# Optimization experiments

Measured on AMD Instinct MI355X. Metric: run time of the kernel, lower is better.

The kernel has to match this reference:

```python
import jax, jax.numpy as jnp
import numpy as np
import itertools

EPS = 1e-3  # BatchNorm1d eps in the original module
N_VOX = 100000


def _build_sparse_structure():
    """Build realistic clustered voxel coords, a 3x3x3 submanifold neighbor
    table (spconv rulebook equivalent), and the unique-merge mapping used by
    sum_duplicates. All index structure is constant (non-differentiable)."""
    rng = np.random.default_rng(0)
    B, Z, Y, X = 2, 40, 1600, 1408  # sparse_shape = grid_size[::-1] + [1,0,0]
    offs01 = np.array(list(itertools.product([0, 1], repeat=3)), dtype=np.int64)
    coords = []
    for b in range(B):
        base = np.stack([rng.integers(0, Z - 1, 13000),
                         rng.integers(0, Y - 1, 13000),
                         rng.integers(0, X - 1, 13000)], 1)
        exp = (base[:, None, :] + offs01[None]).reshape(-1, 3)  # clustered voxels
        coords.append(np.concatenate([np.full((len(exp), 1), b, np.int64), exp], 1))
    coords = np.unique(np.concatenate(coords, 0), axis=0)[:N_VOX]
    assert len(coords) == N_VOX
    # lexicographic unique order => encoded keys are sorted ascending
    key = ((coords[:, 0] * Z + coords[:, 1]) * Y + coords[:, 2]) * X + coords[:, 3]
    offs27 = np.array(list(itertools.product([-1, 0, 1], repeat=3)), np.int64)
    nc = coords[:, None, 1:] + offs27[None]  # [N,27,3]
    inb = (nc >= 0).all(-1) & (nc[..., 0] < Z) & (nc[..., 1] < Y) & (nc[..., 2] < X)
    nk = ((coords[:, None, 0] * Z + nc[..., 0]) * Y + nc[..., 1]) * X + nc[..., 2]
    pos = np.searchsorted(key, nk).clip(0, N_VOX - 1)
    valid = inb & (key[pos] == nk)
    nbr_idx = np.where(valid, pos, -1).astype(np.int32)  # [N,27], -1 = empty
    # second sparse tensor: half its voxels coincide, half are shifted in x
    coords2 = coords.copy()
    coords2[::2, 3] = np.minimum(coords2[::2, 3] + 1, X - 1)
    comb = np.concatenate([coords, coords2], 0)
    uniq, inv = np.unique(comb, axis=0, return_inverse=True)
    return nbr_idx, inv.astype(np.int32), int(len(uniq))


def setup_inputs() -> dict:
    nbr_idx, seg_ids, num_segments = _build_sparse_structure()
    key = jax.random.key(0)
    ks = jax.random.split(key, 6)
    C = 16
    return {
        'voxel_features': jax.random.normal(ks[0], (N_VOX, C), jnp.float32),
        'feat2': jax.random.normal(ks[1], (N_VOX, C), jnp.float32),
        'W0': jax.random.normal(ks[2], (27, C, 16), jnp.float32) * 0.1,
        'g0': jnp.ones((16,), jnp.float32),
        'b0': jnp.zeros((16,), jnp.float32),
        'W1': jax.random.normal(ks[3], (27, 16, 16), jnp.float32) * 0.1,
        'g1': jnp.ones((16,), jnp.float32),
        'b1': jnp.zeros((16,), jnp.float32),
        'Wobo': jax.random.normal(ks[4], (16, 16), jnp.float32) * 0.1,
        'bobo': jnp.zeros((16,), jnp.float32),
        'Wf': jax.random.normal(ks[5], (16, 128), jnp.float32) * 0.1,
        'bf': jnp.zeros((128,), jnp.float32),
        'nbr_idx': jnp.asarray(nbr_idx),
        'seg_ids': jnp.asarray(seg_ids),
        'num_segments': num_segments,
    }


def _subm_bn_relu(x, W, g, b, nbr_idx):
    """Submanifold 3x3x3 sparse conv (gather->GEMM) + BatchNorm1d + ReLU."""
    N = x.shape[0]
    xp = jnp.concatenate([x, jnp.zeros((1, x.shape[1]), x.dtype)], 0)  # pad row
    idx = jnp.where(nbr_idx < 0, N, nbr_idx)  # missing neighbor -> zero row
    y = jnp.einsum('nkc,kco->no', xp[idx], W)  # [N,27,Cin] x [27,Cin,Cout]
    mu = y.mean(0)
    var = y.var(0)
    return jax.nn.relu((y - mu) * jax.lax.rsqrt(var + EPS) * g + b)


def reference(voxel_features, feat2, W0, g0, b0, W1, g1, b1, Wobo, bobo, Wf, bf,
              nbr_idx, seg_ids, num_segments):
    # level-0 conv_input + conv1 (subm conv, BN, ReLU)
    h = _subm_bn_relu(voxel_features, W0, g0, b0, nbr_idx)
    h = _subm_bn_relu(h, W1, g1, b1, nbr_idx)
    # obo_* 1x1 sparse conv on the second branch (plain matmul + bias)
    t2 = feat2 @ Wobo + bobo
    # sum_duplicates: merge coincident sparse indices by summing features
    comb = jnp.concatenate([h, t2], 0)  # [2N,16]
    merged = jax.ops.segment_sum(comb, seg_ids, num_segments=num_segments)
    # final 1x1 sparse conv
    return merged @ Wf + bf  # [U,128]
```

## Files before the change

kernel.cpp:

```cpp
#include <hip/hip_runtime.h>

#define BN_EPS 1e-3f
#define STATC  32
#define MBLK   128

using bfrag  = __attribute__((ext_vector_type(8))) short;
using f32x4v = __attribute__((ext_vector_type(4))) float;
using i32x4v = __attribute__((ext_vector_type(4))) int;

__device__ __forceinline__ unsigned short f2bf(float f) {
    union { float f; unsigned u; } v; v.f = f;
    unsigned r = v.u + 0x7FFFu + ((v.u >> 16) & 1u);
    return (unsigned short)(r >> 16);
}

__global__ __launch_bounds__(256)
void prep_kernel(const float* __restrict__ vf,
                 const float* __restrict__ W0, const float* __restrict__ W1,
                 const float* __restrict__ Wf, const int* __restrict__ seg,
                 unsigned short* __restrict__ xb0,
                 unsigned short* __restrict__ Wb0, unsigned short* __restrict__ Wb1,
                 unsigned short* __restrict__ Wfb,
                 float* __restrict__ stats,
                 int* __restrict__ hidx, int* __restrict__ t2s, int N)
{
    int t = blockIdx.x * 256 + threadIdx.x;
    int TA = 2 * (N + 1);
    unsigned short tmp[8];
    if (t < TA) {
        int n = t >> 1, h = t & 1;
        if (n < N) {
            const f32x4v* yr = (const f32x4v*)(vf + (size_t)n * 16 + h * 8);
            f32x4v v0 = __builtin_nontemporal_load(yr);
            f32x4v v1 = __builtin_nontemporal_load(yr + 1);
#pragma unroll
            for (int j = 0; j < 4; ++j) { tmp[j] = f2bf(v0[j]); tmp[4 + j] = f2bf(v1[j]); }
        } else {
#pragma unroll
            for (int j = 0; j < 8; ++j) tmp[j] = 0;
        }
        *(int4*)(xb0 + (size_t)n * 16 + h * 8) = *(int4*)tmp;
        return;
    }
    t -= TA;
    if (t < 2 * 14 * 64) {
        int w = t >= 896;
        int l = t - w * 896;
        int s = l >> 6, lane = l & 63;
        int q = lane >> 4, n = lane & 15;
        int tap = 2 * s + (q >> 1);
        int cb  = (q & 1) * 8;
        const float* W = w ? W1 : W0;
        unsigned short* Wb = w ? Wb1 : Wb0;
#pragma unroll
        for (int j = 0; j < 8; ++j)
            tmp[j] = (tap < 27) ? f2bf(W[((size_t)(tap * 16 + cb + j)) * 16 + n]) : 0;
        *(int4*)(Wb + (size_t)l * 8) = *(int4*)tmp;
        return;
    }
    t -= 2 * 14 * 64;
    if (t < 512) {
        int ct = t >> 6, lane = t & 63;
        int q = lane >> 4, n = lane & 15;
#pragma unroll
        for (int j = 0; j < 8; ++j)
            tmp[j] = (q < 2) ? f2bf(Wf[(size_t)(q * 8 + j) * 128 + ct * 16 + n]) : 0;
        *(int4*)(Wfb + (size_t)t * 8) = *(int4*)tmp;
        return;
    }
    t -= 512;
    if (t < 2 * STATC * 32) { stats[t] = 0.f; return; }
    t -= 2 * STATC * 32;
    if (t < N) { hidx[seg[t]] = t; return; }
    t -= N;
    if (t < N) {
        int s = seg[N + t];
        if (t == 0 || seg[N + t - 1] != s) t2s[s] = t;
    }
}

__global__ __launch_bounds__(256)
void conv_stats_kernel(const unsigned short* __restrict__ xb,
                       const unsigned short* __restrict__ Wb,
                       const int* __restrict__ nbr,
                       float* __restrict__ y,
                       float* __restrict__ statsC,
                       int N)
{
    __shared__ __align__(16) int   sNbr[64 * 27];
    __shared__ __align__(16) float sY[64 * 16];
    __shared__ float sred[32];
    int tid = threadIdx.x;
    if (tid < 32) sred[tid] = 0.f;

    int gb = blockIdx.x * 1728;
    int NT = N * 27;
    if (gb + 1728 <= NT) {
#pragma unroll
        for (int i = 0; i < 2; ++i) {
            int t4 = i * 256 + tid;
            if (t4 < 432) {
                i32x4v v = __builtin_nontemporal_load((const i32x4v*)(nbr + gb) + t4);
                *(i32x4v*)(sNbr + t4 * 4) = v;
            }
        }
    } else {
#pragma unroll
        for (int i = 0; i < 7; ++i) {
            int t = i * 256 + tid;
            if (t < 1728) {
                int g2 = gb + t;
                sNbr[t] = (g2 < NT) ? __builtin_nontemporal_load(nbr + g2) : -1;
            }
        }
    }
    __syncthreads();

    int lane = tid & 63, wib = tid >> 6;
    int q = lane >> 4, m = lane & 15;
    int c0   = (q & 1) * 8;
    int tpar = q >> 1;
    int lvox = wib * 16 + m;

    int idx[14];
#pragma unroll
    for (int s = 0; s < 14; ++s) {
        int tap = 2 * s + tpar;
        int id  = (tap < 27) ? sNbr[lvox * 27 + tap] : -1;
        idx[s]  = (id >= 0) ? id : N;
    }

    f32x4v acc = {0.f, 0.f, 0.f, 0.f};
#pragma unroll
    for (int s = 0; s < 14; ++s) {
        bfrag a = *(const bfrag*)(xb + (size_t)idx[s] * 16 + c0);
        bfrag b = *(const bfrag*)(Wb + ((size_t)s * 64 + lane) * 8);
        acc = __builtin_amdgcn_mfma_f32_16x16x32_bf16(a, b, acc, 0, 0, 0);
    }

    int o = lane & 15;
#pragma unroll
    for (int i = 0; i < 4; ++i)
        sY[(wib * 16 + q * 4 + i) * 16 + o] = acc[i];

    float s  = acc[0] + acc[1] + acc[2] + acc[3];
    float qq = acc[0] * acc[0] + acc[1] * acc[1] + acc[2] * acc[2] + acc[3] * acc[3];
    s  += __shfl_xor(s, 16);  s  += __shfl_xor(s, 32);
    qq += __shfl_xor(qq, 16); qq += __shfl_xor(qq, 32);
    if (lane < 16) {
        atomicAdd(&sred[lane], s);
        atomicAdd(&sred[16 + lane], qq);
    }
    __syncthreads();

    {
        int row = blockIdx.x * 64 + (tid >> 2);
        if (row < N)
            *(f32x4v*)(y + (size_t)row * 16 + (tid & 3) * 4) =
                *(const f32x4v*)(sY + (size_t)(tid >> 2) * 16 + (tid & 3) * 4);
    }
    if (tid < 32)
        atomicAdd(&statsC[(blockIdx.x & (STATC - 1)) * 32 + tid], sred[tid]);
}

__global__ __launch_bounds__(256)
void bnrelu_cvt_kernel(const float* __restrict__ y0, const float* __restrict__ statsC,
                       const float* __restrict__ g, const float* __restrict__ b,
                       float invN, unsigned short* __restrict__ xb, int N)
{
    __shared__ float sred[32];
    __shared__ float sSc[16], sSh[16];
    int tid = threadIdx.x;
    if (tid < 32) {
        float v = 0.f;
#pragma unroll
        for (int k = 0; k < STATC; ++k) v += statsC[k * 32 + tid];
        sred[tid] = v;
    }
    __syncthreads();
    if (tid < 16) {
        float mu  = sred[tid] * invN;
        float var = sred[16 + tid] * invN - mu * mu;
        float sc  = g[tid] * rsqrtf(var + BN_EPS);
        sSc[tid] = sc;
        sSh[tid] = b[tid] - mu * sc;
    }
    __syncthreads();

    int t = blockIdx.x * 256 + tid;
    if (t >= (N + 1) * 2) return;
    int n = t >> 1, h = t & 1;
    unsigned short tmp[8];
    if (n < N) {
        const f32x4v* yr4 = (const f32x4v*)(y0 + (size_t)n * 16 + h * 8);
        f32x4v v0 = __builtin_nontemporal_load(yr4);
        f32x4v v1 = __builtin_nontemporal_load(yr4 + 1);
#pragma unroll
        for (int j = 0; j < 4; ++j) {
            int c = h * 8 + j;
            tmp[j]     = f2bf(fmaxf(fmaf(v0[j], sSc[c], sSh[c]), 0.f));
            tmp[4 + j] = f2bf(fmaxf(fmaf(v1[j], sSc[c + 4], sSh[c + 4]), 0.f));
        }
    } else {
#pragma unroll
        for (int j = 0; j < 8; ++j) tmp[j] = 0;
    }
    *(int4*)(xb + (size_t)n * 16 + h * 8) = *(int4*)tmp;
}

__global__ __launch_bounds__(256)
void merge_final_kernel(const float* __restrict__ y1, const float* __restrict__ statsC,
                        const float* __restrict__ g, const float* __restrict__ b,
                        float invN,
                        const float* __restrict__ feat2, const float* __restrict__ Wobo,
                        const float* __restrict__ bobo,
                        const int* __restrict__ seg,
                        const int* __restrict__ hidx, const int* __restrict__ t2s,
                        const unsigned short* __restrict__ Wfb,
                        const float* __restrict__ bf,
                        float* __restrict__ out, int N, int U)
{
    __shared__ unsigned short smA[MBLK * 16];
    __shared__ float sred[32];
    __shared__ float sSc[16], sSh[16];
    int tid = threadIdx.x;
    int u0  = blockIdx.x * MBLK;

    if (tid < 32) {
        float v = 0.f;
#pragma unroll
        for (int k = 0; k < STATC; ++k) v += statsC[k * 32 + tid];
        sred[tid] = v;
    }
    __syncthreads();
    if (tid < 16) {
        float mu  = sred[tid] * invN;
        float var = sred[16 + tid] * invN - mu * mu;
        float sc  = g[tid] * rsqrtf(var + BN_EPS);
        sSc[tid] = sc;
        sSh[tid] = b[tid] - mu * sc;
    }
    __syncthreads();

    {
        int sl = tid >> 1, half = tid & 1;
        int u  = u0 + sl;
        bool valid = u < U;
        int uc = valid ? u : 0;
        int hi = hidx[uc];
        int r  = t2s[uc];
        bool hasH = valid && (unsigned)hi < (unsigned)N && seg[hi] == u;
        bool hasT = valid && (unsigned)r  < (unsigned)N && seg[N + r] == u;

        size_t hoff = (size_t)(hasH ? hi : 0) * 16 + half * 8;
        f32x4v yv0 = *(const f32x4v*)(y1 + hoff);
        f32x4v yv1 = *(const f32x4v*)(y1 + hoff + 4);

        float m[8];
#pragma unroll
        for (int j = 0; j < 8; ++j) m[j] = 0.f;
        if (hasH) {
#pragma unroll
            for (int j = 0; j < 4; ++j) {
                int c = half * 8 + j;
                m[j]     = fmaxf(fmaf(yv0[j], sSc[c],     sSh[c]),     0.f);
                m[4 + j] = fmaxf(fmaf(yv1[j], sSc[c + 4], sSh[c + 4]), 0.f);
            }
        }
        if (hasT) {
            float S[16];
#pragma unroll
            for (int c = 0; c < 16; ++c) S[c] = 0.f;
            do {
                const f32x4v* fr = (const f32x4v*)(feat2 + (size_t)r * 16);
                f32x4v f0 = __builtin_nontemporal_load(fr);
                f32x4v f1 = __builtin_nontemporal_load(fr + 1);
                f32x4v f2 = __builtin_nontemporal_load(fr + 2);
                f32x4v f3 = __builtin_nontemporal_load(fr + 3);
#pragma unroll
                for (int c = 0; c < 4; ++c) {
                    S[c] += f0[c]; S[4 + c] += f1[c];
                    S[8 + c] += f2[c]; S[12 + c] += f3[c];
                }
                ++r;
            } while (r < N && seg[N + r] == u);
            float a2[8];
#pragma unroll
            for (int j = 0; j < 8; ++j) a2[j] = bobo[half * 8 + j];
#pragma unroll
            for (int c = 0; c < 16; ++c) {
                float xc = S[c];
                const float* wr = Wobo + c * 16 + half * 8;
#pragma unroll
                for (int j = 0; j < 8; ++j) a2[j] = fmaf(xc, wr[j], a2[j]);
            }
#pragma unroll
            for (int j = 0; j < 8; ++j) m[j] += a2[j];
        }
        unsigned short tb[8];
#pragma unroll
        for (int j = 0; j < 8; ++j) tb[j] = f2bf(m[j]);
        *(int4*)(smA + (size_t)tid * 8) = *(int4*)tb;
    }
    __syncthreads();

    int lane = tid & 63, w = tid >> 6;
    int q = lane >> 4, n = lane & 15;
#pragma unroll
    for (int rt = 0; rt < 2; ++rt) {
        int row0 = w * 32 + rt * 16;
        bfrag a = {0, 0, 0, 0, 0, 0, 0, 0};
        if (q < 2)
            a = *(const bfrag*)(smA + ((size_t)(row0 + n) * 16 + q * 8));
#pragma unroll
        for (int ct = 0; ct < 8; ++ct) {
            bfrag bb = *(const bfrag*)(Wfb + ((size_t)(ct * 64 + lane)) * 8);
            f32x4v acc = {0.f, 0.f, 0.f, 0.f};
            acc = __builtin_amdgcn_mfma_f32_16x16x32_bf16(a, bb, acc, 0, 0, 0);
            int col = ct * 16 + n;
            float bv = bf[col];
#pragma unroll
            for (int i = 0; i < 4; ++i) {
                int u = u0 + row0 + q * 4 + i;
                if (u < U) out[(size_t)u * 128 + col] = acc[i] + bv;
            }
        }
    }
}

extern "C" void kernel_launch(void* const* d_in, const int* in_sizes, int n_in,
                              void* d_out, int out_size, void* d_ws, size_t ws_size,
                              hipStream_t stream)
{
    const float* vf    = (const float*)d_in[0];
    const float* feat2 = (const float*)d_in[1];
    const float* W0    = (const float*)d_in[2];
    const float* g0    = (const float*)d_in[3];
    const float* b0    = (const float*)d_in[4];
    const float* W1    = (const float*)d_in[5];
    const float* g1    = (const float*)d_in[6];
    const float* b1    = (const float*)d_in[7];
    const float* Wobo  = (const float*)d_in[8];
    const float* bobo  = (const float*)d_in[9];
    const float* Wf    = (const float*)d_in[10];
    const float* bf    = (const float*)d_in[11];
    const int*   nbr   = (const int*)d_in[12];
    const int*   seg   = (const int*)d_in[13];

    int N = in_sizes[0] / 16;
    int U = out_size / 128;

    float* out = (float*)d_out;
    float* ws  = (float*)d_ws;

    int gbConv = (N + 63) / 64;

    float* y0     = ws;
    float* y1     = y0 + (size_t)N * 16;
    float* statsA = y1 + (size_t)N * 16;
    float* statsB = statsA + STATC * 32;
    unsigned short* xb0 = (unsigned short*)(statsB + STATC * 32);
    unsigned short* xb1 = xb0 + (size_t)(N + 1) * 16;
    unsigned short* Wb0 = xb1 + (size_t)(N + 1) * 16;
    unsigned short* Wb1 = Wb0 + 14 * 64 * 8;
    unsigned short* Wfb = Wb1 + 14 * 64 * 8;
    int* hidx = (int*)(Wfb + 8 * 64 * 8);
    int* t2s  = hidx + U;

    float invN  = 1.f / (float)N;
    int thrPrep = 2 * (N + 1) + 2 * 14 * 64 + 512 + 2 * STATC * 32 + 2 * N;
    int gbPrep  = (thrPrep + 255) / 256;
    int gbCvt   = ((N + 1) * 2 + 255) / 256;
    int gbMerge = (U + MBLK - 1) / MBLK;

    prep_kernel<<<gbPrep, 256, 0, stream>>>(vf, W0, W1, Wf, seg, xb0, Wb0, Wb1,
                                            Wfb, statsA, hidx, t2s, N);
    conv_stats_kernel<<<gbConv, 256, 0, stream>>>(xb0, Wb0, nbr, y0, statsA, N);
    bnrelu_cvt_kernel<<<gbCvt, 256, 0, stream>>>(y0, statsA, g0, b0, invN, xb1, N);
    conv_stats_kernel<<<gbConv, 256, 0, stream>>>(xb1, Wb1, nbr, y1, statsB, N);
    merge_final_kernel<<<gbMerge, 256, 0, stream>>>(y1, statsB, g1, b1, invN,
                                                    feat2, Wobo, bobo, seg,
                                                    hidx, t2s, Wfb, bf, out, N, U);
}
```

Measured before the change: 150.0 us.

## Pre-swizzle neighbor table into per-lane MFMA order in prep kernel

The prep kernel now rewrites the neighbor index table once into a tiled layout matching each lane's MFMA tap order, with missing neighbors already mapped to the zero row. Both conv kernels then load their 16 indices with four vector loads instead of staging the raw table through shared memory and a barrier. This removes per-conv LDS staging and remapping work, and the raw table is read once instead of twice. In exchange it adds an extra workspace buffer and a write pass in prep, and it leaves a now-unneeded __syncthreads in the conv kernel.

Measured after the change: 156.2 us. 4.2% more time.

```diff
diff --git a/kernel.cpp b/kernel.cpp
--- a/kernel.cpp
+++ b/kernel.cpp
@@ -14,15 +14,18 @@
     return (unsigned short)(r >> 16);
 }
 
+
 __global__ __launch_bounds__(256)
 void prep_kernel(const float* __restrict__ vf,
                  const float* __restrict__ W0, const float* __restrict__ W1,
                  const float* __restrict__ Wf, const int* __restrict__ seg,
+                 const int* __restrict__ nbr,
                  unsigned short* __restrict__ xb0,
                  unsigned short* __restrict__ Wb0, unsigned short* __restrict__ Wb1,
                  unsigned short* __restrict__ Wfb,
                  float* __restrict__ stats,
-                 int* __restrict__ hidx, int* __restrict__ t2s, int N)
+                 int* __restrict__ hidx, int* __restrict__ t2s,
+                 int* __restrict__ nbr2, int nTile, int N)
 {
     int t = blockIdx.x * 256 + threadIdx.x;
     int TA = 2 * (N + 1);
@@ -76,59 +79,57 @@
     if (t < N) {
         int s = seg[N + t];
         if (t == 0 || seg[N + t - 1] != s) t2s[s] = t;
+        return;
+    }
+    t -= N;
+    if (t < nTile * 512) {
+        int lane32 = t & 31;
+        int tpar = lane32 >> 4, m = lane32 & 15;
+        int r2 = t >> 5;
+        int k = r2 & 3; r2 >>= 2;
+        int wib = r2 & 3; int blk = r2 >> 2;
+        int row = blk * 64 + wib * 16 + m;
+        int vals[4];
+#pragma unroll
+        for (int j = 0; j < 4; ++j) {
+            int tap = 8 * k + 2 * j + tpar;
+            int id = -1;
+            if (row < N && tap < 27)
+                id = __builtin_nontemporal_load(nbr + (size_t)row * 27 + tap);
+            vals[j] = (id >= 0) ? id : N;
+        }
+        *(int4*)(nbr2 + (size_t)t * 4) = *(int4*)vals;
     }
 }
 
 __global__ __launch_bounds__(256)
 void conv_stats_kernel(const unsigned short* __restrict__ xb,
                        const unsigned short* __restrict__ Wb,
-                       const int* __restrict__ nbr,
+                       const int* __restrict__ nbr2,
                        float* __restrict__ y,
                        float* __restrict__ statsC,
                        int N)
 {
-    __shared__ __align__(16) int   sNbr[64 * 27];
     __shared__ __align__(16) float sY[64 * 16];
     __shared__ float sred[32];
     int tid = threadIdx.x;
     if (tid < 32) sred[tid] = 0.f;
 
-    int gb = blockIdx.x * 1728;
-    int NT = N * 27;
-    if (gb + 1728 <= NT) {
-#pragma unroll
-        for (int i = 0; i < 2; ++i) {
-            int t4 = i * 256 + tid;
-            if (t4 < 432) {
-                i32x4v v = __builtin_nontemporal_load((const i32x4v*)(nbr + gb) + t4);
-                *(i32x4v*)(sNbr + t4 * 4) = v;
-            }
-        }
-    } else {
-#pragma unroll
-        for (int i = 0; i < 7; ++i) {
-            int t = i * 256 + tid;
-            if (t < 1728) {
-                int g2 = gb + t;
-                sNbr[t] = (g2 < NT) ? __builtin_nontemporal_load(nbr + g2) : -1;
-            }
-        }
-    }
-    __syncthreads();
-
     int lane = tid & 63, wib = tid >> 6;
     int q = lane >> 4, m = lane & 15;
     int c0   = (q & 1) * 8;
     int tpar = q >> 1;
-    int lvox = wib * 16 + m;
-
-    int idx[14];
-#pragma unroll
-    for (int s = 0; s < 14; ++s) {
-        int tap = 2 * s + tpar;
-        int id  = (tap < 27) ? sNbr[lvox * 27 + tap] : -1;
-        idx[s]  = (id >= 0) ? id : N;
-    }
+
+    const int* nb = nbr2 +
+        ((((size_t)blockIdx.x * 4 + wib) * 4) * 32 + tpar * 16 + m) * 4;
+    int idx[16];
+#pragma unroll
+    for (int k = 0; k < 4; ++k) {
+        i32x4v v = *(const i32x4v*)(nb + (size_t)k * 128);
+        idx[4 * k + 0] = v[0]; idx[4 * k + 1] = v[1];
+        idx[4 * k + 2] = v[2]; idx[4 * k + 3] = v[3];
+    }
+    __syncthreads();
 
     f32x4v acc = {0.f, 0.f, 0.f, 0.f};
 #pragma unroll
@@ -353,7 +354,7 @@
     float* out = (float*)d_out;
     float* ws  = (float*)d_ws;
 
-    int gbConv = (N + 63) / 64;
+    int nTile = (N + 63) / 64;
 
     float* y0     = ws;
     float* y1     = y0 + (size_t)N * 16;
@@ -366,18 +367,20 @@
     unsigned short* Wfb = Wb1 + 14 * 64 * 8;
     int* hidx = (int*)(Wfb + 8 * 64 * 8);
     int* t2s  = hidx + U;
+    int* nbr2 = t2s + U;
 
     float invN  = 1.f / (float)N;
-    int thrPrep = 2 * (N + 1) + 2 * 14 * 64 + 512 + 2 * STATC * 32 + 2 * N;
-    int gbPrep  = (thrPrep + 255) / 256;
+    long thrPrep = 2L * (N + 1) + 2 * 14 * 64 + 512 + 2 * STATC * 32 + 2L * N
+                 + (long)nTile * 512;
+    int gbPrep  = (int)((thrPrep + 255) / 256);
     int gbCvt   = ((N + 1) * 2 + 255) / 256;
     int gbMerge = (U + MBLK - 1) / MBLK;
 
-    prep_kernel<<<gbPrep, 256, 0, stream>>>(vf, W0, W1, Wf, seg, xb0, Wb0, Wb1,
-                                            Wfb, statsA, hidx, t2s, N);
-    conv_stats_kernel<<<gbConv, 256, 0, stream>>>(xb0, Wb0, nbr, y0, statsA, N);
+    prep_kernel<<<gbPrep, 256, 0, stream>>>(vf, W0, W1, Wf, seg, nbr, xb0, Wb0, Wb1,
+                                            Wfb, statsA, hidx, t2s, nbr2, nTile, N);
+    conv_stats_kernel<<<nTile, 256, 0, stream>>>(xb0, Wb0, nbr2, y0, statsA, N);
     bnrelu_cvt_kernel<<<gbCvt, 256, 0, stream>>>(y0, statsA, g0, b0, invN, xb1, N);
-    conv_stats_kernel<<<gbConv, 256, 0, stream>>>(xb1, Wb1, nbr, y1, statsB, N);
+    conv_stats_kernel<<<nTile, 256, 0, stream>>>(xb1, Wb1, nbr2, y1, statsB, N);
     merge_final_kernel<<<gbMerge, 256, 0, stream>>>(y1, statsB, g1, b1, invN,
                                                     feat2, Wobo, bobo, seg,
                                                     hidx, t2s, Wfb, bf, out, N, U);
```
